# Performance work log

Measured on AMD Instinct MI355X. Metric: run time of the kernel, lower is better.

Reference implementation:

```python
import jax, jax.numpy as jnp
import numpy as np

TOPK = 2
EPS = float(np.finfo(np.float64).eps)


def setup_inputs() -> dict:
    key = jax.random.key(0)
    ks = jax.random.split(key, 6)
    B, D, E = 8192, 1024, 8
    x = jax.random.normal(ks[0], (B, D), dtype=jnp.float32)
    noise = jax.random.normal(ks[1], (B, E), dtype=jnp.float32)
    w_gate = jax.random.normal(ks[2], (D, E), dtype=jnp.float32) * 0.02
    w_noise = jax.random.normal(ks[3], (D, E), dtype=jnp.float32) * 0.02
    W_experts = jax.random.normal(ks[4], (E, D, D), dtype=jnp.float32) * 0.02
    b_experts = jax.random.normal(ks[5], (E, D), dtype=jnp.float32) * 0.02
    return {"x": x, "noise": noise, "w_gate": w_gate, "w_noise": w_noise,
            "W_experts": W_experts, "b_experts": b_experts}


def _gates(x, w_gate, w_noise, noise):
    # noisy top-k gating (Shazeer et al.)
    clean_logits = x @ w_gate                                  # [B, E]
    noise_stddev = jax.nn.softplus(x @ w_noise) + 0.01         # [B, E]
    logits = clean_logits + noise * noise_stddev               # [B, E]
    E = logits.shape[1]
    top_logits, top_idx = jax.lax.top_k(logits, min(TOPK + 1, E))
    top_k_logits = top_logits[:, :TOPK]
    top_k_idx = top_idx[:, :TOPK]
    top_k_gates = jax.nn.softmax(top_k_logits, axis=1)         # [B, k]
    B = logits.shape[0]
    gates = jnp.zeros_like(logits).at[jnp.arange(B)[:, None], top_k_idx].set(top_k_gates)
    return gates                                               # [B, E] sparse


def reference(x, noise, w_gate, w_noise, W_experts, b_experts):
    gates = _gates(x, w_gate, w_noise, noise)                  # [B, E]
    # dense equivalent of sort-based dispatch/combine: zero gates mask out
    # unselected experts, so the combined result is identical math.
    expert_out = jnp.einsum("bd,edh->beh", x, W_experts) + b_experts[None]  # [B, E, D]
    combined = jnp.einsum("be,beh->bh", gates, jnp.exp(expert_out))         # [B, D]
    combined = jnp.where(combined == 0, EPS, combined)
    return jnp.log(combined)
```

## Files before the change

### kernel.cpp

```cpp
#include <hip/hip_runtime.h>
#include <hip/hip_bf16.h>
#include <math.h>

#define B_ROWS 8192
#define DDIM   1024
#define NEXP   8

typedef __attribute__((ext_vector_type(8))) __bf16 bf16x8;
typedef __attribute__((ext_vector_type(4))) float  f32x4;

__device__ __forceinline__ unsigned short f2bf(float f) {
    unsigned u = __builtin_bit_cast(unsigned, f);
    u = (u + 0x7fffu + ((u >> 16) & 1u)) >> 16;
    return (unsigned short)u;
}

#define GLOAD_LDS16(gptr, lptr)                                                \
    __builtin_amdgcn_global_load_lds(                                          \
        (const __attribute__((address_space(1))) unsigned int*)(gptr),         \
        (__attribute__((address_space(3))) unsigned int*)(lptr), 16, 0, 0)

__global__ __launch_bounds__(256) void xconv_kernel(
    const float* __restrict__ x, __hip_bfloat16* __restrict__ xbf)
{
    int i = blockIdx.x * 256 + threadIdx.x;
    const int stride = gridDim.x * 256;
    const int n8 = B_ROWS * DDIM / 8;
    for (; i < n8; i += stride) {
        const float4 f0 = *(const float4*)(x + (size_t)i * 8);
        const float4 f1 = *(const float4*)(x + (size_t)i * 8 + 4);
        union { bf16x8 v; unsigned short u[8]; } pk;
        pk.u[0] = f2bf(f0.x); pk.u[1] = f2bf(f0.y); pk.u[2] = f2bf(f0.z); pk.u[3] = f2bf(f0.w);
        pk.u[4] = f2bf(f1.x); pk.u[5] = f2bf(f1.y); pk.u[6] = f2bf(f1.z); pk.u[7] = f2bf(f1.w);
        *(bf16x8*)((__hip_bfloat16*)xbf + (size_t)i * 8) = pk.v;
    }
}

__global__ __launch_bounds__(256) void wtrans_kernel(
    const float* __restrict__ W, __hip_bfloat16* __restrict__ Wt)
{
    const int e  = blockIdx.z;
    const int k0 = blockIdx.y * 64;
    const int n0 = blockIdx.x * 64;
    __shared__ float st[64][65];

    const int t = threadIdx.x;
    {
        const int kk = t >> 4;
        const int nn = (t & 15) * 4;
#pragma unroll
        for (int p = 0; p < 4; ++p) {
            const int k = p * 16 + kk;
            const float4 v = *(const float4*)(W + (size_t)e * DDIM * DDIM
                                                + (size_t)(k0 + k) * DDIM + n0 + nn);
            st[k][nn + 0] = v.x; st[k][nn + 1] = v.y;
            st[k][nn + 2] = v.z; st[k][nn + 3] = v.w;
        }
    }
    __syncthreads();
    {
        const int wave = t >> 6, lane = t & 63;
        const int nr = lane >> 3, kc = lane & 7;
#pragma unroll
        for (int p = 0; p < 2; ++p) {
            const int n = p * 32 + wave * 8 + nr;
            union { bf16x8 v; unsigned short u[8]; } pk;
#pragma unroll
            for (int j = 0; j < 8; ++j) pk.u[j] = f2bf(st[kc * 8 + j][n]);
            *(bf16x8*)((__hip_bfloat16*)Wt + (size_t)e * DDIM * DDIM
                        + (size_t)(n0 + n) * DDIM + k0 + kc * 8) = pk.v;
        }
    }
}

__global__ __launch_bounds__(256) void gating_kernel(
    const float* __restrict__ x, const float* __restrict__ noise,
    const float* __restrict__ w_gate, const float* __restrict__ w_noise,
    int* __restrict__ counts, int* __restrict__ rowlist, float* __restrict__ gatelist)
{
    __shared__ float wtab[DDIM][16];

    const int t = threadIdx.x;
    {
        const int k0 = t * 4;
#pragma unroll
        for (int kk = 0; kk < 4; ++kk) {
            const float4 g0 = *(const float4*)(w_gate  + (size_t)(k0 + kk) * NEXP);
            const float4 g1 = *(const float4*)(w_gate  + (size_t)(k0 + kk) * NEXP + 4);
            const float4 n0 = *(const float4*)(w_noise + (size_t)(k0 + kk) * NEXP);
            const float4 n1 = *(const float4*)(w_noise + (size_t)(k0 + kk) * NEXP + 4);
            *(float4*)&wtab[k0 + kk][0]  = g0;
            *(float4*)&wtab[k0 + kk][4]  = g1;
            *(float4*)&wtab[k0 + kk][8]  = n0;
            *(float4*)&wtab[k0 + kk][12] = n1;
        }
    }
    __syncthreads();

    const int wave = t >> 6, lane = t & 63;
    const int rs = lane >> 4, c = lane & 15;
    const int row = (blockIdx.x * 4 + wave) * 4 + rs;

    double acc = 0.0;
    const float* xr = x + (size_t)row * DDIM;
#pragma unroll 4
    for (int k4 = 0; k4 < DDIM / 4; ++k4) {
        const float4 xv = *(const float4*)(xr + k4 * 4);
        acc += (double)(xv.x * wtab[k4 * 4 + 0][c]);
        acc += (double)(xv.y * wtab[k4 * 4 + 1][c]);
        acc += (double)(xv.z * wtab[k4 * 4 + 2][c]);
        acc += (double)(xv.w * wtab[k4 * 4 + 3][c]);
    }

    const double vnoise = __shfl_xor(acc, 8);

    double lgv = -1.0e300;
    if (c < 8) {
        const double z  = vnoise;
        const double sp = (z > 30.0) ? z : log1p(exp(z));
        lgv = acc + (double)noise[(size_t)row * NEXP + c] * (sp + 0.01);
    }

    double bv = lgv; int bi = c;
#pragma unroll
    for (int off = 1; off <= 4; off <<= 1) {
        const double ov = __shfl_xor(bv, off);
        const int    oi = __shfl_xor(bi, off);
        if (ov > bv || (ov == bv && oi < bi)) { bv = ov; bi = oi; }
    }
    double b2v = (c == bi) ? -1.0e300 : lgv; int b2i = c;
#pragma unroll
    for (int off = 1; off <= 4; off <<= 1) {
        const double ov = __shfl_xor(b2v, off);
        const int    oi = __shfl_xor(b2i, off);
        if (ov > b2v || (ov == b2v && oi < b2i)) { b2v = ov; b2i = oi; }
    }

    if (c == 0) {
        const double g0 = 1.0 / (1.0 + exp(b2v - bv));
        const double g1 = 1.0 - g0;
        int p0 = atomicAdd(&counts[bi], 1);
        rowlist [bi * B_ROWS + p0] = row;
        gatelist[bi * B_ROWS + p0] = (float)g0;
        int p1 = atomicAdd(&counts[b2i], 1);
        rowlist [b2i * B_ROWS + p1] = (int)((unsigned)row | 0x80000000u);
        gatelist[b2i * B_ROWS + p1] = (float)g1;
    }
}

__global__ __launch_bounds__(256) void moe_gemm_kernel(
    const __hip_bfloat16* __restrict__ xbf, const __hip_bfloat16* __restrict__ Wt,
    const float* __restrict__ bias,
    const int* __restrict__ counts, const int* __restrict__ rowlist,
    const float* __restrict__ gatelist, float* __restrict__ out, float* __restrict__ out2)
{
    const int nt = blockIdx.x;
    const int e  = blockIdx.y;
    const int mt = blockIdx.z;
    const int cnt  = counts[e];
    const int row0 = mt * 128;
    if (row0 >= cnt) return;

    __shared__ int   srow[128];
    __shared__ unsigned char srank[128];
    __shared__ float sgate[128];
    __shared__ __align__(16) unsigned char Alds[128 * 128];
    __shared__ __align__(16) unsigned char Blds[128 * 128];

    const int t = threadIdx.x;
    if (t < 128) {
        const int r = row0 + t;
        const unsigned er = (r < cnt) ? (unsigned)rowlist[e * B_ROWS + r] : 0u;
        srow[t]  = (int)(er & 0x7fffffffu);
        srank[t] = (unsigned char)(er >> 31);
        sgate[t] = (r < cnt) ? gatelist[e * B_ROWS + r] : 0.0f;
    }
    __syncthreads();

    const int wave = t >> 6, lane = t & 63;
    const int wr = wave >> 1, wc = wave & 1;
    const int l4 = lane >> 4, l16 = lane & 15;
    const int lrow  = lane >> 3;
    const int lchunk = (lane & 7) ^ lrow;

    const char* asrc[4]; const char* bsrc[4];
#pragma unroll
    for (int i = 0; i < 4; ++i) {
        const int r  = wave * 32 + i * 8 + lrow;
        asrc[i] = (const char*)xbf + 2 * ((size_t)srow[r] * DDIM + lchunk * 8);
        const int gn = nt * 128 + wave * 32 + i * 8 + lrow;
        bsrc[i] = (const char*)Wt  + 2 * ((size_t)e * DDIM * DDIM + (size_t)gn * DDIM + lchunk * 8);
    }

    f32x4 acc[4][4];
#pragma unroll
    for (int m = 0; m < 4; ++m)
#pragma unroll
        for (int n = 0; n < 4; ++n) acc[m][n] = (f32x4){0.f, 0.f, 0.f, 0.f};

    for (int kt = 0; kt < DDIM / 64; ++kt) {
        const int koff = kt * 128;
#pragma unroll
        for (int i = 0; i < 4; ++i) {
            GLOAD_LDS16(asrc[i] + koff, Alds + (wave * 32 + i * 8) * 128);
            GLOAD_LDS16(bsrc[i] + koff, Blds + (wave * 32 + i * 8) * 128);
        }
        asm volatile("s_waitcnt vmcnt(0)" ::: "memory");
        __syncthreads();

#pragma unroll
        for (int ks = 0; ks < 2; ++ks) {
            bf16x8 af[4], bfr[4];
#pragma unroll
            for (int m = 0; m < 4; ++m) {
                const int row = wr * 64 + m * 16 + l16;
                af[m] = *(const bf16x8*)(Alds + row * 128 + ((ks * 64 + l4 * 16) ^ ((row & 7) << 4)));
            }
#pragma unroll
            for (int n = 0; n < 4; ++n) {
                const int rn = wc * 64 + n * 16 + l16;
                bfr[n] = *(const bf16x8*)(Blds + rn * 128 + ((ks * 64 + l4 * 16) ^ ((rn & 7) << 4)));
            }
#pragma unroll
            for (int m = 0; m < 4; ++m)
#pragma unroll
                for (int n = 0; n < 4; ++n)
                    acc[m][n] = __builtin_amdgcn_mfma_f32_16x16x32_bf16(af[m], bfr[n], acc[m][n], 0, 0, 0);
        }
        __syncthreads();
    }

#pragma unroll
    for (int m = 0; m < 4; ++m) {
#pragma unroll
        for (int n = 0; n < 4; ++n) {
#pragma unroll
            for (int j = 0; j < 4; ++j) {
                const int R = wr * 64 + m * 16 + l4 * 4 + j;
                if (row0 + R < cnt) {
                    const int   brow = srow[R];
                    const float g    = sgate[R];
                    const int   h    = nt * 128 + wc * 64 + n * 16 + l16;
                    const float v    = g * __expf(acc[m][n][j] + bias[e * DDIM + h]);
                    float* dst = srank[R] ? out2 : out;
                    dst[(size_t)brow * DDIM + h] = v;
                }
            }
        }
    }
}

__global__ __launch_bounds__(256) void logeps_kernel(
    float* __restrict__ o, const float* __restrict__ o2, int n4)
{
    const float EPSF = 2.220446049250313e-16f;
    int i = blockIdx.x * blockDim.x + threadIdx.x;
    const int stride = gridDim.x * blockDim.x;
    float4* p = (float4*)o;
    const float4* q = (const float4*)o2;
    for (; i < n4; i += stride) {
        float4 a = p[i];
        const float4 b = q[i];
        a.x += b.x; a.y += b.y; a.z += b.z; a.w += b.w;
        a.x = __logf(a.x == 0.0f ? EPSF : a.x);
        a.y = __logf(a.y == 0.0f ? EPSF : a.y);
        a.z = __logf(a.z == 0.0f ? EPSF : a.z);
        a.w = __logf(a.w == 0.0f ? EPSF : a.w);
        p[i] = a;
    }
}

extern "C" void kernel_launch(void* const* d_in, const int* in_sizes, int n_in,
                              void* d_out, int out_size, void* d_ws, size_t ws_size,
                              hipStream_t stream)
{
    const float* x       = (const float*)d_in[0];
    const float* noise   = (const float*)d_in[1];
    const float* w_gate  = (const float*)d_in[2];
    const float* w_noise = (const float*)d_in[3];
    const float* W       = (const float*)d_in[4];
    const float* bias    = (const float*)d_in[5];
    float* out = (float*)d_out;

    char* ws = (char*)d_ws;
    int*   counts   = (int*)ws;
    int*   rowlist  = (int*)(ws + 1024);
    float* gatelist = (float*)(ws + 1024 + NEXP * B_ROWS * 4);
    __hip_bfloat16* xbf = (__hip_bfloat16*)(ws + (1u << 20));
    __hip_bfloat16* Wt  = (__hip_bfloat16*)(ws + (1u << 20) + (16u << 20));
    float* out2 = (float*)(ws + (1u << 20) + (32u << 20));

    hipMemsetAsync(counts, 0, 64, stream);

    xconv_kernel<<<1024, 256, 0, stream>>>(x, xbf);
    wtrans_kernel<<<dim3(16, 16, NEXP), 256, 0, stream>>>(W, Wt);
    gating_kernel<<<B_ROWS / 16, 256, 0, stream>>>(x, noise, w_gate, w_noise,
                                                   counts, rowlist, gatelist);

    dim3 grid(NEXP , NEXP , B_ROWS / 128 );
    moe_gemm_kernel<<<grid, 256, 0, stream>>>(xbf, Wt, bias, counts, rowlist, gatelist,
                                              out, out2);

    logeps_kernel<<<2048, 256, 0, stream>>>(out, out2, out_size / 4);
}
```

Before: 323.5 us.

## Double-buffer MoE GEMM LDS tiles and restructure gating weight access

The expert GEMM now uses two LDS buffers, so the global-to-LDS load for the next K tile is issued before the MFMAs on the current tile, hiding load latency behind compute. The gating kernel drops its per-block 64KB LDS weight table. A new small kernel transposes w_gate and w_noise into a k-contiguous layout, and gating reads it with float4 loads into eight independent double accumulators. Launch order is also changed. The double buffer doubles LDS per block to 64KB, which may lower occupancy, and the split accumulators change the summation order in gating.

```diff
diff --git a/kernel.cpp b/kernel.cpp
--- a/kernel.cpp
+++ b/kernel.cpp
@@ -73,44 +73,46 @@
     }
 }
 
+__global__ __launch_bounds__(256) void wprep_kernel(
+    const float* __restrict__ wg, const float* __restrict__ wn, float* __restrict__ wt)
+{
+    const int t = blockIdx.x * 256 + threadIdx.x;
+    if (t < 16 * DDIM) {
+        const int c = t >> 10, k = t & 1023;
+        wt[t] = (c < 8) ? wg[k * NEXP + c] : wn[k * NEXP + (c - 8)];
+    }
+}
+
 __global__ __launch_bounds__(256) void gating_kernel(
     const float* __restrict__ x, const float* __restrict__ noise,
-    const float* __restrict__ w_gate, const float* __restrict__ w_noise,
+    const float* __restrict__ wt,
     int* __restrict__ counts, int* __restrict__ rowlist, float* __restrict__ gatelist)
 {
-    __shared__ float wtab[DDIM][16];
-
     const int t = threadIdx.x;
-    {
-        const int k0 = t * 4;
-#pragma unroll
-        for (int kk = 0; kk < 4; ++kk) {
-            const float4 g0 = *(const float4*)(w_gate  + (size_t)(k0 + kk) * NEXP);
-            const float4 g1 = *(const float4*)(w_gate  + (size_t)(k0 + kk) * NEXP + 4);
-            const float4 n0 = *(const float4*)(w_noise + (size_t)(k0 + kk) * NEXP);
-            const float4 n1 = *(const float4*)(w_noise + (size_t)(k0 + kk) * NEXP + 4);
-            *(float4*)&wtab[k0 + kk][0]  = g0;
-            *(float4*)&wtab[k0 + kk][4]  = g1;
-            *(float4*)&wtab[k0 + kk][8]  = n0;
-            *(float4*)&wtab[k0 + kk][12] = n1;
-        }
-    }
-    __syncthreads();
-
     const int wave = t >> 6, lane = t & 63;
     const int rs = lane >> 4, c = lane & 15;
     const int row = (blockIdx.x * 4 + wave) * 4 + rs;
 
-    double acc = 0.0;
-    const float* xr = x + (size_t)row * DDIM;
+    const float* xr = x  + (size_t)row * DDIM;
+    const float* wr = wt + (size_t)c * DDIM;
+
+    double a0 = 0, a1 = 0, a2 = 0, a3 = 0, a4 = 0, a5 = 0, a6 = 0, a7 = 0;
 #pragma unroll 4
-    for (int k4 = 0; k4 < DDIM / 4; ++k4) {
-        const float4 xv = *(const float4*)(xr + k4 * 4);
-        acc += (double)(xv.x * wtab[k4 * 4 + 0][c]);
-        acc += (double)(xv.y * wtab[k4 * 4 + 1][c]);
-        acc += (double)(xv.z * wtab[k4 * 4 + 2][c]);
-        acc += (double)(xv.w * wtab[k4 * 4 + 3][c]);
-    }
+    for (int k8 = 0; k8 < DDIM / 8; ++k8) {
+        const float4 xv0 = *(const float4*)(xr + k8 * 8);
+        const float4 xv1 = *(const float4*)(xr + k8 * 8 + 4);
+        const float4 wv0 = *(const float4*)(wr + k8 * 8);
+        const float4 wv1 = *(const float4*)(wr + k8 * 8 + 4);
+        a0 += (double)(xv0.x * wv0.x);
+        a1 += (double)(xv0.y * wv0.y);
+        a2 += (double)(xv0.z * wv0.z);
+        a3 += (double)(xv0.w * wv0.w);
+        a4 += (double)(xv1.x * wv1.x);
+        a5 += (double)(xv1.y * wv1.y);
+        a6 += (double)(xv1.z * wv1.z);
+        a7 += (double)(xv1.w * wv1.w);
+    }
+    const double acc = ((a0 + a1) + (a2 + a3)) + ((a4 + a5) + (a6 + a7));
 
     const double vnoise = __shfl_xor(acc, 8);
 
@@ -164,8 +166,8 @@
     __shared__ int   srow[128];
     __shared__ unsigned char srank[128];
     __shared__ float sgate[128];
-    __shared__ __align__(16) unsigned char Alds[128 * 128];
-    __shared__ __align__(16) unsigned char Blds[128 * 128];
+    __shared__ __align__(16) unsigned char Alds[2][128 * 128];
+    __shared__ __align__(16) unsigned char Blds[2][128 * 128];
 
     const int t = threadIdx.x;
     if (t < 128) {
@@ -198,15 +200,22 @@
 #pragma unroll
         for (int n = 0; n < 4; ++n) acc[m][n] = (f32x4){0.f, 0.f, 0.f, 0.f};
 
+#define STAGE(bufi, koff)                                                      \
+    {                                                                          \
+        _Pragma("unroll")                                                      \
+        for (int i = 0; i < 4; ++i) {                                          \
+            GLOAD_LDS16(asrc[i] + (koff), Alds[bufi] + (wave * 32 + i * 8) * 128); \
+            GLOAD_LDS16(bsrc[i] + (koff), Blds[bufi] + (wave * 32 + i * 8) * 128); \
+        }                                                                      \
+    }
+
+    STAGE(0, 0)
+    asm volatile("s_waitcnt vmcnt(0)" ::: "memory");
+    __builtin_amdgcn_s_barrier();
+
+    int cur = 0;
     for (int kt = 0; kt < DDIM / 64; ++kt) {
-        const int koff = kt * 128;
-#pragma unroll
-        for (int i = 0; i < 4; ++i) {
-            GLOAD_LDS16(asrc[i] + koff, Alds + (wave * 32 + i * 8) * 128);
-            GLOAD_LDS16(bsrc[i] + koff, Blds + (wave * 32 + i * 8) * 128);
-        }
-        asm volatile("s_waitcnt vmcnt(0)" ::: "memory");
-        __syncthreads();
+        if (kt < DDIM / 64 - 1) STAGE(cur ^ 1, (kt + 1) * 128)
 
 #pragma unroll
         for (int ks = 0; ks < 2; ++ks) {
@@ -214,12 +223,12 @@
 #pragma unroll
             for (int m = 0; m < 4; ++m) {
                 const int row = wr * 64 + m * 16 + l16;
-                af[m] = *(const bf16x8*)(Alds + row * 128 + ((ks * 64 + l4 * 16) ^ ((row & 7) << 4)));
+                af[m] = *(const bf16x8*)(Alds[cur] + row * 128 + ((ks * 64 + l4 * 16) ^ ((row & 7) << 4)));
             }
 #pragma unroll
             for (int n = 0; n < 4; ++n) {
                 const int rn = wc * 64 + n * 16 + l16;
-                bfr[n] = *(const bf16x8*)(Blds + rn * 128 + ((ks * 64 + l4 * 16) ^ ((rn & 7) << 4)));
+                bfr[n] = *(const bf16x8*)(Blds[cur] + rn * 128 + ((ks * 64 + l4 * 16) ^ ((rn & 7) << 4)));
             }
 #pragma unroll
             for (int m = 0; m < 4; ++m)
@@ -227,8 +236,12 @@
                 for (int n = 0; n < 4; ++n)
                     acc[m][n] = __builtin_amdgcn_mfma_f32_16x16x32_bf16(af[m], bfr[n], acc[m][n], 0, 0, 0);
         }
-        __syncthreads();
-    }
+
+        asm volatile("s_waitcnt vmcnt(0)" ::: "memory");
+        __builtin_amdgcn_s_barrier();
+        cur ^= 1;
+    }
+#undef STAGE
 
 #pragma unroll
     for (int m = 0; m < 4; ++m) {
@@ -284,18 +297,20 @@
 
     char* ws = (char*)d_ws;
     int*   counts   = (int*)ws;
-    int*   rowlist  = (int*)(ws + 1024);
-    float* gatelist = (float*)(ws + 1024 + NEXP * B_ROWS * 4);
+    float* wt       = (float*)(ws + 256);
+    int*   rowlist  = (int*)(ws + 256 + 65536);
+    float* gatelist = (float*)(ws + 256 + 65536 + NEXP * B_ROWS * 4);
     __hip_bfloat16* xbf = (__hip_bfloat16*)(ws + (1u << 20));
     __hip_bfloat16* Wt  = (__hip_bfloat16*)(ws + (1u << 20) + (16u << 20));
     float* out2 = (float*)(ws + (1u << 20) + (32u << 20));
 
     hipMemsetAsync(counts, 0, 64, stream);
 
+    wprep_kernel<<<64, 256, 0, stream>>>(w_gate, w_noise, wt);
+    gating_kernel<<<B_ROWS / 16, 256, 0, stream>>>(x, noise, wt,
+                                                   counts, rowlist, gatelist);
     xconv_kernel<<<1024, 256, 0, stream>>>(x, xbf);
     wtrans_kernel<<<dim3(16, 16, NEXP), 256, 0, stream>>>(W, Wt);
-    gating_kernel<<<B_ROWS / 16, 256, 0, stream>>>(x, noise, w_gate, w_noise,
-                                                   counts, rowlist, gatelist);
 
     dim3 grid(NEXP , NEXP , B_ROWS / 128 );
     moe_gemm_kernel<<<grid, 256, 0, stream>>>(xbf, Wt, bias, counts, rowlist, gatelist,
```

Result: slower. 382.8 us (+18.3%).
